# Optimization experiments

Measured on AMD Instinct MI355X. Metric: run time of the kernel, lower is better.

## Reference

```python
import jax, jax.numpy as jnp
import numpy as np

HIDDEN = 1024

def setup_inputs() -> dict:
    key = jax.random.key(0)
    k1, k2, k3 = jax.random.split(key, 3)
    X = jax.random.normal(k1, (4, 2048, HIDDEN), dtype=jnp.float32)
    W = jax.random.normal(k2, (HIDDEN, 3 * HIDDEN), dtype=jnp.float32) * (1.0 / np.sqrt(HIDDEN))
    b = jax.random.normal(k3, (3 * HIDDEN,), dtype=jnp.float32) * 0.02
    return {"X": X, "W": W, "b": b}

def reference(X, W, b):
    D = X.shape[-1]
    # fused QKV projection: [B,S,3D]
    QKV = jnp.einsum('bsd,de->bse', X, W) + b
    Q, K, V = jnp.split(QKV, 3, axis=-1)
    # full attention scores [B,S,S]
    scores = jnp.einsum('bqd,bkd->bqk', Q, K) / jnp.sqrt(jnp.float32(D))
    attn = jax.nn.softmax(scores, axis=-1)
    out = jnp.einsum('bqk,bkd->bqd', attn, V)
    return out
```

## Files before the change

kernel.cpp:

```cpp
#include <hip/hip_runtime.h>

typedef unsigned short u16;
typedef unsigned int   u32;
typedef __attribute__((ext_vector_type(8)))  short bf16x8;
typedef __attribute__((ext_vector_type(16))) float f32x16;
typedef __attribute__((ext_vector_type(4)))  unsigned short us4;

__device__ __forceinline__ u16 f2bf(float f) {
    union { float f; u32 u; } v; v.f = f;
    u32 u = v.u;
    return (u16)((u + 0x7fffu + ((u >> 16) & 1u)) >> 16);
}
__device__ __forceinline__ float bf2f_lo(u32 p) {
    union { u32 u; float f; } t; t.u = p << 16; return t.f;
}
__device__ __forceinline__ float bf2f_hi(u32 p) {
    union { u32 u; float f; } t; t.u = p & 0xffff0000u; return t.f;
}

__device__ __forceinline__ void gload_lds16(const void* g, void* l) {
    __builtin_amdgcn_global_load_lds((const __attribute__((address_space(1))) u32*)g,
                                     (__attribute__((address_space(3))) u32*)l,
                                     16, 0, 0);
}

template<bool OUT_BF16, bool ADD_BIAS, bool VT_OUT, int MODE>
__global__ __launch_bounds__(256, 2)
void gemm256(const u16* __restrict__ A, int lda, size_t strA,
             const u16* __restrict__ B, int ldb, size_t strB,
             void* __restrict__ Cv, int ldc, size_t strC,
             const float* __restrict__ bias, int K, float alpha)
{
    __shared__ __align__(16) u16 As[2][256 * 32];
    __shared__ __align__(16) u16 Bs[2][128 * 32];

    const int tid  = threadIdx.x;
    const int w    = tid >> 6;
    const int lane = tid & 63;
    const int wm   = w >> 1, wn = w & 1;
    const int l31  = lane & 31, lh = lane >> 5;

    const u32 id = blockIdx.x, x = id & 7, j = id >> 3;
    int mb, nb, bb;
    if (MODE == 0) { bb = 0;             mb = 8 * (int)(j & 3) + (int)x;        nb = (int)(j >> 2); }
    else           { bb = (int)(x >> 1); mb = 2 * (int)(j & 3) + (int)(x & 1);  nb = (int)(j >> 2); }
    const int m0 = mb * 256, n0 = nb * 128;

    A += (size_t)bb * strA;
    B += (size_t)bb * strB;

    size_t goffA[4], goffB[2];
#pragma unroll
    for (int h = 0; h < 4; ++h) {
        const int c = h * 256 + w * 64 + lane;
        const int r = c >> 2;
        const int q = ((c & 3) - (r >> 1)) & 3;
        goffA[h] = (size_t)(m0 + r) * lda + q * 8;
    }
#pragma unroll
    for (int h = 0; h < 2; ++h) {
        const int c = h * 256 + w * 64 + lane;
        const int r = c >> 2;
        const int q = ((c & 3) - (r >> 1)) & 3;
        goffB[h] = (size_t)(n0 + r) * ldb + q * 8;
    }

    int offA[4][2], offB[2][2];
#pragma unroll
    for (int i = 0; i < 4; ++i) {
        const int ra = wm * 128 + i * 32 + l31;
#pragma unroll
        for (int ks = 0; ks < 2; ++ks)
            offA[i][ks] = (ra * 4 + ((ks * 2 + lh + (ra >> 1)) & 3)) * 16;
    }
#pragma unroll
    for (int jj = 0; jj < 2; ++jj) {
        const int rb = wn * 64 + jj * 32 + l31;
#pragma unroll
        for (int ks = 0; ks < 2; ++ks)
            offB[jj][ks] = (rb * 4 + ((ks * 2 + lh + (rb >> 1)) & 3)) * 16;
    }

    f32x16 acc[4][2] = {};

#pragma unroll
    for (int h = 0; h < 4; ++h)
        gload_lds16(A + goffA[h], (char*)As[0] + (h * 256 + w * 64) * 16);
#pragma unroll
    for (int h = 0; h < 2; ++h)
        gload_lds16(B + goffB[h], (char*)Bs[0] + (h * 256 + w * 64) * 16);

    int cur = 0;
    for (int k0 = 0; k0 < K; k0 += 32) {
        __syncthreads();

        const int nk = k0 + 32;
        if (nk < K) {
#pragma unroll
            for (int h = 0; h < 4; ++h)
                gload_lds16(A + goffA[h] + nk, (char*)As[cur ^ 1] + (h * 256 + w * 64) * 16);
#pragma unroll
            for (int h = 0; h < 2; ++h)
                gload_lds16(B + goffB[h] + nk, (char*)Bs[cur ^ 1] + (h * 256 + w * 64) * 16);
        }

        const u16* Ac = As[cur]; const u16* Bc = Bs[cur];
#pragma unroll
        for (int ks = 0; ks < 2; ++ks) {
            bf16x8 af[4], bfr[2];
#pragma unroll
            for (int i = 0; i < 4; ++i)
                af[i] = *(const bf16x8*)((const char*)Ac + offA[i][ks]);
#pragma unroll
            for (int jj = 0; jj < 2; ++jj)
                bfr[jj] = *(const bf16x8*)((const char*)Bc + offB[jj][ks]);
#pragma unroll
            for (int i = 0; i < 4; ++i)
#pragma unroll
                for (int jj = 0; jj < 2; ++jj)
                    acc[i][jj] = __builtin_amdgcn_mfma_f32_32x32x16_bf16(
                        af[i], bfr[jj], acc[i][jj], 0, 0, 0);
        }
        cur ^= 1;
    }

    float bval[2];
    if (ADD_BIAS) {
#pragma unroll
        for (int jj = 0; jj < 2; ++jj) bval[jj] = bias[n0 + wn * 64 + jj * 32 + l31];
    }
#pragma unroll
    for (int i = 0; i < 4; ++i) {
        const int rowb = m0 + wm * 128 + i * 32 + 4 * lh;
#pragma unroll
        for (int jj = 0; jj < 2; ++jj) {
            const int col = n0 + wn * 64 + jj * 32 + l31;
            if (VT_OUT) {
                const int b = rowb >> 11;
                u16* dst = (u16*)Cv + ((size_t)(b * 1024) + col) * 2048 + (rowb & 2047);
#pragma unroll
                for (int g = 0; g < 4; ++g) {
                    us4 o = { f2bf(acc[i][jj][4 * g + 0] + bval[jj]),
                              f2bf(acc[i][jj][4 * g + 1] + bval[jj]),
                              f2bf(acc[i][jj][4 * g + 2] + bval[jj]),
                              f2bf(acc[i][jj][4 * g + 3] + bval[jj]) };
                    *(us4*)(dst + 8 * g) = o;
                }
            } else {
#pragma unroll
                for (int r = 0; r < 16; ++r) {
                    const int row = rowb + (r & 3) + 8 * (r >> 2);
                    float v = acc[i][jj][r] * alpha;
                    if (ADD_BIAS) v += bval[jj];
                    if (OUT_BF16)
                        ((u16*)Cv)[(size_t)bb * strC + (size_t)row * ldc + col] = f2bf(v);
                    else
                        ((float*)Cv)[(size_t)bb * strC + (size_t)row * ldc + col] = v;
                }
            }
        }
    }
}

template<bool OUT_BF16>
__global__ __launch_bounds__(256)
void gemm128(const u16* __restrict__ A, int lda, size_t strA,
             const u16* __restrict__ B, int ldb, size_t strB,
             void* __restrict__ Cv, int ldc, size_t strC,
             int K, float alpha)
{
    __shared__ __align__(16) u16 As[2][128 * 32];
    __shared__ __align__(16) u16 Bs[2][128 * 32];

    const int tid  = threadIdx.x;
    const int w    = tid >> 6;
    const int lane = tid & 63;
    const int wm   = w >> 1, wn = w & 1;
    const int l31  = lane & 31, lh = lane >> 5;

    const u32 id = blockIdx.x, x = id & 7, j = id >> 3;
    const int bb = (int)(x >> 1);
    const int mb = 2 * (int)(j & 7) + (int)(x & 1);
    const int nb = (int)(j >> 3);
    const int m0 = mb * 128, n0 = nb * 128;

    A += (size_t)bb * strA;
    B += (size_t)bb * strB;

    size_t goffA[2], goffB[2];
#pragma unroll
    for (int h = 0; h < 2; ++h) {
        const int c = h * 256 + w * 64 + lane;
        const int r = c >> 2;
        const int q = ((c & 3) - (r >> 1)) & 3;
        goffA[h] = (size_t)(m0 + r) * lda + q * 8;
        goffB[h] = (size_t)(n0 + r) * ldb + q * 8;
    }

    int offA[2][2], offB[2][2];
#pragma unroll
    for (int i = 0; i < 2; ++i) {
        const int ra = wm * 64 + i * 32 + l31;
        const int rb = wn * 64 + i * 32 + l31;
#pragma unroll
        for (int ks = 0; ks < 2; ++ks) {
            const int qq = ks * 2 + lh;
            offA[i][ks] = (ra * 4 + ((qq + (ra >> 1)) & 3)) * 16;
            offB[i][ks] = (rb * 4 + ((qq + (rb >> 1)) & 3)) * 16;
        }
    }

    f32x16 acc[2][2] = {};

#pragma unroll
    for (int h = 0; h < 2; ++h) {
        gload_lds16(A + goffA[h], (char*)As[0] + (h * 256 + w * 64) * 16);
        gload_lds16(B + goffB[h], (char*)Bs[0] + (h * 256 + w * 64) * 16);
    }

    int cur = 0;
    for (int k0 = 0; k0 < K; k0 += 32) {
        __syncthreads();

        const int nk = k0 + 32;
        if (nk < K) {
#pragma unroll
            for (int h = 0; h < 2; ++h) {
                gload_lds16(A + goffA[h] + nk, (char*)As[cur ^ 1] + (h * 256 + w * 64) * 16);
                gload_lds16(B + goffB[h] + nk, (char*)Bs[cur ^ 1] + (h * 256 + w * 64) * 16);
            }
        }

        const u16* Ac = As[cur]; const u16* Bc = Bs[cur];
#pragma unroll
        for (int ks = 0; ks < 2; ++ks) {
            bf16x8 af[2], bfr[2];
#pragma unroll
            for (int i = 0; i < 2; ++i) {
                af[i]  = *(const bf16x8*)((const char*)Ac + offA[i][ks]);
                bfr[i] = *(const bf16x8*)((const char*)Bc + offB[i][ks]);
            }
#pragma unroll
            for (int i = 0; i < 2; ++i)
#pragma unroll
                for (int jj = 0; jj < 2; ++jj)
                    acc[i][jj] = __builtin_amdgcn_mfma_f32_32x32x16_bf16(
                        af[i], bfr[jj], acc[i][jj], 0, 0, 0);
        }
        cur ^= 1;
    }

#pragma unroll
    for (int i = 0; i < 2; ++i) {
        const int rowb = m0 + wm * 64 + i * 32 + 4 * lh;
#pragma unroll
        for (int jj = 0; jj < 2; ++jj) {
            const int col = n0 + wn * 64 + jj * 32 + l31;
#pragma unroll
            for (int r = 0; r < 16; ++r) {
                const int row = rowb + (r & 3) + 8 * (r >> 2);
                float v = acc[i][jj][r] * alpha;
                if (OUT_BF16)
                    ((u16*)Cv)[(size_t)bb * strC + (size_t)row * ldc + col] = f2bf(v);
                else
                    ((float*)Cv)[(size_t)bb * strC + (size_t)row * ldc + col] = v;
            }
        }
    }
}

__global__ __launch_bounds__(256)
void convert_x(const float* __restrict__ X, u16* __restrict__ Xb, int n4)
{
    int i = blockIdx.x * blockDim.x + threadIdx.x;
    if (i < n4) {
        float4 v = ((const float4*)X)[i];
        us4 o = { f2bf(v.x), f2bf(v.y), f2bf(v.z), f2bf(v.w) };
        ((us4*)Xb)[i] = o;
    }
}

__global__ __launch_bounds__(256)
void transpose_w(const float* __restrict__ W, u16* __restrict__ Wt)
{
    __shared__ u16 t[64][65];
    const int k0 = blockIdx.x * 64, n0 = blockIdx.y * 64;
    const int tx = threadIdx.x, ty = threadIdx.y;
#pragma unroll
    for (int i = 0; i < 64; i += 4)
        t[ty + i][tx] = f2bf(W[(size_t)(k0 + ty + i) * 3072 + n0 + tx]);
    __syncthreads();
#pragma unroll
    for (int i = 0; i < 64; i += 4)
        Wt[(size_t)(n0 + ty + i) * 1024 + k0 + tx] = t[tx][ty + i];
}

__global__ __launch_bounds__(256)
void softmax_rows(u16* __restrict__ S)
{
    __shared__ float redm[4], reds[4];
    u16* sr = S + (size_t)blockIdx.x * 2048;
    const int t = threadIdx.x;

    uint4 raw = ((const uint4*)sr)[t];
    float xx[8];
    xx[0] = bf2f_lo(raw.x); xx[1] = bf2f_hi(raw.x);
    xx[2] = bf2f_lo(raw.y); xx[3] = bf2f_hi(raw.y);
    xx[4] = bf2f_lo(raw.z); xx[5] = bf2f_hi(raw.z);
    xx[6] = bf2f_lo(raw.w); xx[7] = bf2f_hi(raw.w);

    float mx = fmaxf(fmaxf(fmaxf(xx[0], xx[1]), fmaxf(xx[2], xx[3])),
                     fmaxf(fmaxf(xx[4], xx[5]), fmaxf(xx[6], xx[7])));
#pragma unroll
    for (int o = 32; o; o >>= 1) mx = fmaxf(mx, __shfl_xor(mx, o));
    if ((t & 63) == 0) redm[t >> 6] = mx;
    __syncthreads();
    mx = fmaxf(fmaxf(redm[0], redm[1]), fmaxf(redm[2], redm[3]));

    float e[8], s = 0.f;
#pragma unroll
    for (int k = 0; k < 8; ++k) { e[k] = __expf(xx[k] - mx); s += e[k]; }
#pragma unroll
    for (int o = 32; o; o >>= 1) s += __shfl_xor(s, o);
    if ((t & 63) == 0) reds[t >> 6] = s;
    __syncthreads();
    s = reds[0] + reds[1] + reds[2] + reds[3];
    const float inv = 1.0f / s;

    uint4 o4;
    o4.x = (u32)f2bf(e[0] * inv) | ((u32)f2bf(e[1] * inv) << 16);
    o4.y = (u32)f2bf(e[2] * inv) | ((u32)f2bf(e[3] * inv) << 16);
    o4.z = (u32)f2bf(e[4] * inv) | ((u32)f2bf(e[5] * inv) << 16);
    o4.w = (u32)f2bf(e[6] * inv) | ((u32)f2bf(e[7] * inv) << 16);
    ((uint4*)sr)[t] = o4;
}

extern "C" void kernel_launch(void* const* d_in, const int* in_sizes, int n_in,
                              void* d_out, int out_size, void* d_ws, size_t ws_size,
                              hipStream_t stream)
{
    const float* X    = (const float*)d_in[0];
    const float* W    = (const float*)d_in[1];
    const float* bias = (const float*)d_in[2];
    float* out = (float*)d_out;
    char* ws = (char*)d_ws;

    u16* QK = (u16*)ws;
    u16* Vt = (u16*)(ws + 33554432);
    u16* S  = (u16*)(ws + 50331648);
    u16* Xb = (u16*)(ws + 50331648);
    u16* Wt = (u16*)(ws + 67108864);

    convert_x<<<8192, 256, 0, stream>>>(X, Xb, 8192 * 1024 / 4);
    transpose_w<<<dim3(16, 48), dim3(64, 4), 0, stream>>>(W, Wt);

    gemm256<true, true, false, 0><<<512, 256, 0, stream>>>(
        Xb, 1024, 0, Wt, 1024, 0, QK, 2048, 0, bias, 1024, 1.0f);

    gemm256<true, true, true, 0><<<256, 256, 0, stream>>>(
        Xb, 1024, 0, Wt + (size_t)2048 * 1024, 1024, 0, Vt, 2048, 0,
        bias + 2048, 1024, 1.0f);

    gemm256<true, false, false, 2><<<512, 256, 0, stream>>>(
        QK,        2048, (size_t)2048 * 2048,
        QK + 1024, 2048, (size_t)2048 * 2048,
        S,         2048, (size_t)2048 * 2048,
        nullptr, 1024, 0.03125f);

    softmax_rows<<<8192, 256, 0, stream>>>(S);

    gemm128<false><<<512, 256, 0, stream>>>(
        S,  2048, (size_t)2048 * 2048,
        Vt, 2048, (size_t)1024 * 2048,
        out, 1024, (size_t)2048 * 1024,
        2048, 1.0f);
}
```

Measured before the change: 279.7 us.

## Merge QKV projection launches and split-K the PV GEMM across two sub-blocks

The Q/K and V projection GEMMs become one 768-block launch. Blocks whose column tile starts at 2048 or beyond write their result transposed into Vt, and occupancy is raised to 3 blocks per CU. The attention-times-V GEMM becomes a 512-thread kernel in which two 256-thread halves each cover half of the K=2048 range. Their partial accumulators are summed through LDS before the fp32 output is stored. This adds parallelism per tile and removes one launch, but drops the double buffering in the PV kernel and adds a reduction step.

```diff
diff --git a/kernel.cpp b/kernel.cpp
--- a/kernel.cpp
+++ b/kernel.cpp
@@ -24,11 +24,12 @@
                                      16, 0, 0);
 }
 
-template<bool OUT_BF16, bool ADD_BIAS, bool VT_OUT, int MODE>
-__global__ __launch_bounds__(256, 2)
+template<int MINW, bool OUT_BF16, bool ADD_BIAS, bool PROJ, int MODE>
+__global__ __launch_bounds__(256, MINW)
 void gemm256(const u16* __restrict__ A, int lda, size_t strA,
              const u16* __restrict__ B, int ldb, size_t strB,
              void* __restrict__ Cv, int ldc, size_t strC,
+             u16* __restrict__ Vtp,
              const float* __restrict__ bias, int K, float alpha)
 {
     __shared__ __align__(16) u16 As[2][256 * 32];
@@ -129,15 +130,16 @@
 #pragma unroll
         for (int jj = 0; jj < 2; ++jj) bval[jj] = bias[n0 + wn * 64 + jj * 32 + l31];
     }
+    const bool vt = PROJ && (n0 >= 2048);
 #pragma unroll
     for (int i = 0; i < 4; ++i) {
         const int rowb = m0 + wm * 128 + i * 32 + 4 * lh;
 #pragma unroll
         for (int jj = 0; jj < 2; ++jj) {
             const int col = n0 + wn * 64 + jj * 32 + l31;
-            if (VT_OUT) {
+            if (vt) {
                 const int b = rowb >> 11;
-                u16* dst = (u16*)Cv + ((size_t)(b * 1024) + col) * 2048 + (rowb & 2047);
+                u16* dst = Vtp + ((size_t)(b * 1024) + (col - 2048)) * 2048 + (rowb & 2047);
 #pragma unroll
                 for (int g = 0; g < 4; ++g) {
                     us4 o = { f2bf(acc[i][jj][4 * g + 0] + bval[jj]),
@@ -162,19 +164,18 @@
     }
 }
 
-template<bool OUT_BF16>
-__global__ __launch_bounds__(256)
-void gemm128(const u16* __restrict__ A, int lda, size_t strA,
-             const u16* __restrict__ B, int ldb, size_t strB,
-             void* __restrict__ Cv, int ldc, size_t strC,
-             int K, float alpha)
-{
-    __shared__ __align__(16) u16 As[2][128 * 32];
-    __shared__ __align__(16) u16 Bs[2][128 * 32];
+__global__ __launch_bounds__(512, 4)
+void gemm128s(const u16* __restrict__ A, int lda, size_t strA,
+              const u16* __restrict__ B, int ldb, size_t strB,
+              float* __restrict__ C, int ldc, size_t strC)
+{
+    __shared__ __align__(16) char smem[65536];
 
     const int tid  = threadIdx.x;
-    const int w    = tid >> 6;
-    const int lane = tid & 63;
+    const int sub  = tid >> 8;
+    const int t    = tid & 255;
+    const int w    = t >> 6;
+    const int lane = t & 63;
     const int wm   = w >> 1, wn = w & 1;
     const int l31  = lane & 31, lh = lane >> 5;
 
@@ -184,13 +185,16 @@
     const int nb = (int)(j >> 3);
     const int m0 = mb * 128, n0 = nb * 128;
 
-    A += (size_t)bb * strA;
-    B += (size_t)bb * strB;
+    A += (size_t)bb * strA + sub * 1024;
+    B += (size_t)bb * strB + sub * 1024;
+
+    u16* As = (u16*)(smem + sub * 16384);
+    u16* Bs = (u16*)(smem + sub * 16384 + 8192);
 
     size_t goffA[2], goffB[2];
 #pragma unroll
     for (int h = 0; h < 2; ++h) {
-        const int c = h * 256 + w * 64 + lane;
+        const int c = h * 256 + t;
         const int r = c >> 2;
         const int q = ((c & 3) - (r >> 1)) & 3;
         goffA[h] = (size_t)(m0 + r) * lda + q * 8;
@@ -212,33 +216,21 @@
 
     f32x16 acc[2][2] = {};
 
-#pragma unroll
-    for (int h = 0; h < 2; ++h) {
-        gload_lds16(A + goffA[h], (char*)As[0] + (h * 256 + w * 64) * 16);
-        gload_lds16(B + goffB[h], (char*)Bs[0] + (h * 256 + w * 64) * 16);
-    }
-
-    int cur = 0;
-    for (int k0 = 0; k0 < K; k0 += 32) {
+    for (int k0 = 0; k0 < 1024; k0 += 32) {
+#pragma unroll
+        for (int h = 0; h < 2; ++h) {
+            gload_lds16(A + goffA[h] + k0, (char*)As + (h * 256 + w * 64) * 16);
+            gload_lds16(B + goffB[h] + k0, (char*)Bs + (h * 256 + w * 64) * 16);
+        }
         __syncthreads();
 
-        const int nk = k0 + 32;
-        if (nk < K) {
-#pragma unroll
-            for (int h = 0; h < 2; ++h) {
-                gload_lds16(A + goffA[h] + nk, (char*)As[cur ^ 1] + (h * 256 + w * 64) * 16);
-                gload_lds16(B + goffB[h] + nk, (char*)Bs[cur ^ 1] + (h * 256 + w * 64) * 16);
-            }
-        }
-
-        const u16* Ac = As[cur]; const u16* Bc = Bs[cur];
 #pragma unroll
         for (int ks = 0; ks < 2; ++ks) {
             bf16x8 af[2], bfr[2];
 #pragma unroll
             for (int i = 0; i < 2; ++i) {
-                af[i]  = *(const bf16x8*)((const char*)Ac + offA[i][ks]);
-                bfr[i] = *(const bf16x8*)((const char*)Bc + offB[i][ks]);
+                af[i]  = *(const bf16x8*)((const char*)As + offA[i][ks]);
+                bfr[i] = *(const bf16x8*)((const char*)Bs + offB[i][ks]);
             }
 #pragma unroll
             for (int i = 0; i < 2; ++i)
@@ -247,23 +239,39 @@
                     acc[i][jj] = __builtin_amdgcn_mfma_f32_32x32x16_bf16(
                         af[i], bfr[jj], acc[i][jj], 0, 0, 0);
         }
-        cur ^= 1;
-    }
-
-#pragma unroll
-    for (int i = 0; i < 2; ++i) {
-        const int rowb = m0 + wm * 64 + i * 32 + 4 * lh;
-#pragma unroll
-        for (int jj = 0; jj < 2; ++jj) {
-            const int col = n0 + wn * 64 + jj * 32 + l31;
-#pragma unroll
-            for (int r = 0; r < 16; ++r) {
-                const int row = rowb + (r & 3) + 8 * (r >> 2);
-                float v = acc[i][jj][r] * alpha;
-                if (OUT_BF16)
-                    ((u16*)Cv)[(size_t)bb * strC + (size_t)row * ldc + col] = f2bf(v);
-                else
-                    ((float*)Cv)[(size_t)bb * strC + (size_t)row * ldc + col] = v;
+        __syncthreads();
+    }
+
+    float* red = (float*)smem;
+    if (sub == 1) {
+#pragma unroll
+        for (int c = 0; c < 16; ++c) {
+            const int i = c >> 3, jj = (c >> 2) & 1, r0 = (c & 3) * 4;
+            float4 v = { acc[i][jj][r0 + 0], acc[i][jj][r0 + 1],
+                         acc[i][jj][r0 + 2], acc[i][jj][r0 + 3] };
+            *(float4*)(red + t * 64 + ((c + t) & 15) * 4) = v;
+        }
+    }
+    __syncthreads();
+    if (sub == 0) {
+#pragma unroll
+        for (int c = 0; c < 16; ++c) {
+            const int i = c >> 3, jj = (c >> 2) & 1, r0 = (c & 3) * 4;
+            float4 v = *(const float4*)(red + t * 64 + ((c + t) & 15) * 4);
+            acc[i][jj][r0 + 0] += v.x; acc[i][jj][r0 + 1] += v.y;
+            acc[i][jj][r0 + 2] += v.z; acc[i][jj][r0 + 3] += v.w;
+        }
+#pragma unroll
+        for (int i = 0; i < 2; ++i) {
+            const int rowb = m0 + wm * 64 + i * 32 + 4 * lh;
+#pragma unroll
+            for (int jj = 0; jj < 2; ++jj) {
+                const int col = n0 + wn * 64 + jj * 32 + l31;
+#pragma unroll
+                for (int r = 0; r < 16; ++r) {
+                    const int row = rowb + (r & 3) + 8 * (r >> 2);
+                    C[(size_t)bb * strC + (size_t)row * ldc + col] = acc[i][jj][r];
+                }
             }
         }
     }
@@ -354,24 +362,19 @@
     convert_x<<<8192, 256, 0, stream>>>(X, Xb, 8192 * 1024 / 4);
     transpose_w<<<dim3(16, 48), dim3(64, 4), 0, stream>>>(W, Wt);
 
-    gemm256<true, true, false, 0><<<512, 256, 0, stream>>>(
-        Xb, 1024, 0, Wt, 1024, 0, QK, 2048, 0, bias, 1024, 1.0f);
-
-    gemm256<true, true, true, 0><<<256, 256, 0, stream>>>(
-        Xb, 1024, 0, Wt + (size_t)2048 * 1024, 1024, 0, Vt, 2048, 0,
-        bias + 2048, 1024, 1.0f);
-
-    gemm256<true, false, false, 2><<<512, 256, 0, stream>>>(
+    gemm256<3, true, true, true, 0><<<768, 256, 0, stream>>>(
+        Xb, 1024, 0, Wt, 1024, 0, QK, 2048, 0, Vt, bias, 1024, 1.0f);
+
+    gemm256<2, true, false, false, 2><<<512, 256, 0, stream>>>(
         QK,        2048, (size_t)2048 * 2048,
         QK + 1024, 2048, (size_t)2048 * 2048,
         S,         2048, (size_t)2048 * 2048,
-        nullptr, 1024, 0.03125f);
+        nullptr, nullptr, 1024, 0.03125f);
 
     softmax_rows<<<8192, 256, 0, stream>>>(S);
 
-    gemm128<false><<<512, 256, 0, stream>>>(
+    gemm128s<<<512, 512, 0, stream>>>(
         S,  2048, (size_t)2048 * 2048,
         Vt, 2048, (size_t)1024 * 2048,
-        out, 1024, (size_t)2048 * 1024,
-        2048, 1.0f);
-}
+        out, 1024, (size_t)2048 * 1024);
+}
```

After: 255.3 us. 1.1x faster.
